# Performance work log

Measured on AMD Instinct MI355X. Metric: run time of the kernel, lower is better.

The kernel has to match this reference:

```python
import jax, jax.numpy as jnp
import numpy as np

B, N = 65536, 128

def setup_inputs() -> dict:
    key = jax.random.key(0)
    k1, k2, k3, k4, k5 = jax.random.split(key, 5)
    density = jax.random.uniform(k1, (B, N), dtype=jnp.float32) * 10.0   # nonneg densities
    deltas = jax.random.uniform(k2, (B, N), dtype=jnp.float32) * 0.05 + 1e-3  # positive step sizes
    zs = jnp.cumsum(deltas, axis=-1) + 2.0                               # monotone sample depths
    raw_rgbs = jax.random.uniform(k4, (B, N, 3), dtype=jnp.float32)
    raw_normals = jax.random.normal(k5, (B, N, 3), dtype=jnp.float32)
    return {"density": density, "deltas": deltas, "zs": zs,
            "raw_rgbs": raw_rgbs, "raw_normals": raw_normals}


def reference(density, deltas, zs, raw_rgbs, raw_normals):
    # alpha -> transmittance (exclusive cumprod) -> weight
    alpha = 1.0 - jnp.exp(-density * deltas)                 # [B, N]
    one_minus = 1.0 - alpha
    cp = jnp.cumprod(one_minus, axis=-1)                     # inclusive cumprod
    trans = jnp.concatenate([jnp.ones_like(cp[:, :1]), cp[:, :-1]], axis=-1)  # exclusive
    weight = alpha * trans                                   # [B, N]

    # composites
    rgb = jnp.einsum('bn,bnc->bc', weight, raw_rgbs)         # [B, 3]
    acc = jnp.sum(weight, axis=1, keepdims=True)             # [B, 1]
    depth = jnp.sum(weight * zs, axis=1, keepdims=True) / (acc + 1e-8)  # normalized
    normal = jnp.einsum('bn,bnc->bc', weight, raw_normals)   # [B, 3]

    # pack outputs: rgb(3) | depth(1) | normal(3) | acc(1) -> [B, 8]
    return jnp.concatenate([rgb, depth, normal, acc], axis=-1)
```

## Files before the change

### kernel.cpp

```cpp
#include <hip/hip_runtime.h>


constexpr int RAYS = 65536;
constexpr int NS   = 128;
constexpr int WPB  = 4;

#define DPP_ADD(x, ctrl, rm)                                                   \
    x += __int_as_float(__builtin_amdgcn_update_dpp(                           \
        0, __float_as_int(x), ctrl, rm, 0xf, true))

__device__ __forceinline__ float scan32(float x) {
    DPP_ADD(x, 0x111, 0xf);
    DPP_ADD(x, 0x112, 0xf);
    DPP_ADD(x, 0x114, 0xf);
    DPP_ADD(x, 0x118, 0xf);
    DPP_ADD(x, 0x142, 0xa);
    return x;
}

__global__ __launch_bounds__(256) void render_composite_kernel(
    const float* __restrict__ density,
    const float* __restrict__ deltas,
    const float* __restrict__ zs,
    const float* __restrict__ rgbs,
    const float* __restrict__ normals,
    float* __restrict__ out)
{
    __shared__ __align__(16) float wlds[WPB][256];

    const int tid  = threadIdx.x;
    const int wv   = tid >> 6;
    const int l    = tid & 63;
    const int k    = l & 31;
    const int half = l >> 5;

    const int ray0 = (blockIdx.x * WPB + wv) * 2;
    const int ray  = ray0 + half;

    const size_t row = (size_t)ray * NS;
    const float4 d  = reinterpret_cast<const float4*>(density + row)[k];
    const float4 dl = reinterpret_cast<const float4*>(deltas  + row)[k];
    const float4 z  = reinterpret_cast<const float4*>(zs      + row)[k];

    const float4* cr = reinterpret_cast<const float4*>(rgbs)    + (size_t)ray0 * 96;
    const float4* cn = reinterpret_cast<const float4*>(normals) + (size_t)ray0 * 96;
    const float4 vr0 = cr[0 * 64 + l];
    const float4 vr1 = cr[1 * 64 + l];
    const float4 vr2 = cr[2 * 64 + l];
    const float4 vn0 = cn[0 * 64 + l];
    const float4 vn1 = cn[1 * 64 + l];
    const float4 vn2 = cn[2 * 64 + l];

    const float s0 = d.x * dl.x;
    const float s1 = d.y * dl.y;
    const float s2 = d.z * dl.z;
    const float s3 = d.w * dl.w;
    const float slocal = (s0 + s1) + (s2 + s3);
    const float prefix = scan32(slocal);
    const float S0 = prefix - slocal;

    const float e0 = __expf(-S0);
    const float e1 = __expf(-(S0 + s0));
    const float e2 = __expf(-(S0 + s0 + s1));
    const float e3 = __expf(-(S0 + s0 + s1 + s2));
    const float e4 = __expf(-(S0 + slocal));
    const float w0 = e0 - e1, w1 = e1 - e2, w2 = e2 - e3, w3 = e3 - e4;

    float acc_w  = (w0 + w1) + (w2 + w3);
    float acc_wz = w0 * z.x + w1 * z.y + w2 * z.z + w3 * z.w;

    reinterpret_cast<float4*>(&wlds[wv][0])[l] = make_float4(w0, w1, w2, w3);
    const float* wbase = &wlds[wv][0];

    float r0c0 = 0.f, r0c1 = 0.f, r0c2 = 0.f;
    float r1c0 = 0.f, r1c1 = 0.f, r1c2 = 0.f;
    float m0c0 = 0.f, m0c1 = 0.f, m0c2 = 0.f;
    float m1c0 = 0.f, m1c1 = 0.f, m1c2 = 0.f;

    auto proc = [](const float4 v, float wA, float wB, int rt,
                   float& c0, float& c1, float& c2) {
        const float q0 = wA * v.x + wB * v.w;
        const float q1 = ((rt == 2) ? wB : wA) * v.y;
        const float q2 = ((rt >= 1) ? wB : wA) * v.z;
        const float a0 = (rt == 0) ? q0 : (rt == 1) ? q2 : q1;
        const float a1 = (rt == 0) ? q1 : (rt == 1) ? q0 : q2;
        const float a2 = (rt == 0) ? q2 : (rt == 1) ? q1 : q0;
        c0 += a0; c1 += a1; c2 += a2;
    };

    #pragma unroll
    for (int t = 0; t < 3; ++t) {
        const int f  = 256 * t + 4 * l;
        const int q  = f / 3;
        const int rt = f - 3 * q;
        const float wA = wbase[q];
        const float wB = wbase[q + 1];
        const float4 vr = (t == 0) ? vr0 : (t == 1) ? vr1 : vr2;
        const float4 vn = (t == 0) ? vn0 : (t == 1) ? vn1 : vn2;

        if (t == 0) {
            proc(vr, wA, wB, rt, r0c0, r0c1, r0c2);
            proc(vn, wA, wB, rt, m0c0, m0c1, m0c2);
        } else if (t == 2) {
            proc(vr, wA, wB, rt, r1c0, r1c1, r1c2);
            proc(vn, wA, wB, rt, m1c0, m1c1, m1c2);
        } else {
            float t0 = 0.f, t1c = 0.f, t2c = 0.f, u0 = 0.f, u1 = 0.f, u2 = 0.f;
            proc(vr, wA, wB, rt, t0, t1c, t2c);
            proc(vn, wA, wB, rt, u0, u1, u2);
            const bool isr0 = (l < 32);
            r0c0 += isr0 ? t0 : 0.f;  r1c0 += isr0 ? 0.f : t0;
            r0c1 += isr0 ? t1c : 0.f; r1c1 += isr0 ? 0.f : t1c;
            r0c2 += isr0 ? t2c : 0.f; r1c2 += isr0 ? 0.f : t2c;
            m0c0 += isr0 ? u0 : 0.f;  m1c0 += isr0 ? 0.f : u0;
            m0c1 += isr0 ? u1 : 0.f;  m1c1 += isr0 ? 0.f : u1;
            m0c2 += isr0 ? u2 : 0.f;  m1c2 += isr0 ? 0.f : u2;
        }
    }

    auto reduce2 = [&](float cR0, float cR1) -> float {
        const float sel = half ? cR1 : cR0;
        const float oth = half ? cR0 : cR1;
        const float m = sel + __shfl_xor(oth, 32, 64);
        return scan32(m);
    };
    const float R  = reduce2(r0c0, r1c0);
    const float G  = reduce2(r0c1, r1c1);
    const float Bc = reduce2(r0c2, r1c2);
    const float NR = reduce2(m0c0, m1c0);
    const float NG = reduce2(m0c1, m1c1);
    const float NB = reduce2(m0c2, m1c2);
    acc_w  = scan32(acc_w);
    acc_wz = scan32(acc_wz);

    if (k == 31) {
        const float depth = acc_wz / (acc_w + 1e-8f);
        float4* o = reinterpret_cast<float4*>(out + (size_t)ray * 8);
        o[0] = make_float4(R, G, Bc, depth);
        o[1] = make_float4(NR, NG, NB, acc_w);
    }
}

extern "C" void kernel_launch(void* const* d_in, const int* in_sizes, int n_in,
                              void* d_out, int out_size, void* d_ws, size_t ws_size,
                              hipStream_t stream) {
    const float* density = (const float*)d_in[0];
    const float* deltas  = (const float*)d_in[1];
    const float* zs      = (const float*)d_in[2];
    const float* rgbs    = (const float*)d_in[3];
    const float* normals = (const float*)d_in[4];
    float* out = (float*)d_out;

    const int grid = RAYS / (WPB * 2);
    render_composite_kernel<<<grid, 256, 0, stream>>>(
        density, deltas, zs, rgbs, normals, out);
}
```

Measured before the change: 279.7 us.

## Process four ray pairs per wave with double-buffered register prefetch

```diff
diff --git a/kernel.cpp b/kernel.cpp
--- a/kernel.cpp
+++ b/kernel.cpp
@@ -4,6 +4,10 @@
 constexpr int RAYS = 65536;
 constexpr int NS   = 128;
 constexpr int WPB  = 4;
+constexpr int NBLOCKS = 2048;
+constexpr int NWAVES  = NBLOCKS * WPB;
+constexpr int PAIRS   = RAYS / 2;
+constexpr int PPW     = PAIRS / NWAVES;
 
 #define DPP_ADD(x, ctrl, rm)                                                   \
     x += __int_as_float(__builtin_amdgcn_update_dpp(                           \
@@ -18,43 +22,37 @@
     return x;
 }
 
-__global__ __launch_bounds__(256) void render_composite_kernel(
-    const float* __restrict__ density,
-    const float* __restrict__ deltas,
-    const float* __restrict__ zs,
-    const float* __restrict__ rgbs,
-    const float* __restrict__ normals,
-    float* __restrict__ out)
+struct Stage {
+    float4 d, dl, z;
+    float4 r0, r1, r2;
+    float4 n0, n1, n2;
+};
+
+__device__ __forceinline__ void stage_load(
+    Stage& s, int pair, int l, int k,
+    const float* __restrict__ density, const float* __restrict__ deltas,
+    const float* __restrict__ zs, const float* __restrict__ rgbs,
+    const float* __restrict__ normals)
 {
-    __shared__ __align__(16) float wlds[WPB][256];
+    const int ray = pair * 2 + (l >> 5);
+    const size_t row = (size_t)ray * NS;
+    s.d  = reinterpret_cast<const float4*>(density + row)[k];
+    s.dl = reinterpret_cast<const float4*>(deltas  + row)[k];
+    s.z  = reinterpret_cast<const float4*>(zs      + row)[k];
+    const float4* cr = reinterpret_cast<const float4*>(rgbs)    + (size_t)pair * 192;
+    const float4* cn = reinterpret_cast<const float4*>(normals) + (size_t)pair * 192;
+    s.r0 = cr[l]; s.r1 = cr[64 + l]; s.r2 = cr[128 + l];
+    s.n0 = cn[l]; s.n1 = cn[64 + l]; s.n2 = cn[128 + l];
+}
 
-    const int tid  = threadIdx.x;
-    const int wv   = tid >> 6;
-    const int l    = tid & 63;
-    const int k    = l & 31;
-    const int half = l >> 5;
-
-    const int ray0 = (blockIdx.x * WPB + wv) * 2;
-    const int ray  = ray0 + half;
-
-    const size_t row = (size_t)ray * NS;
-    const float4 d  = reinterpret_cast<const float4*>(density + row)[k];
-    const float4 dl = reinterpret_cast<const float4*>(deltas  + row)[k];
-    const float4 z  = reinterpret_cast<const float4*>(zs      + row)[k];
-
-    const float4* cr = reinterpret_cast<const float4*>(rgbs)    + (size_t)ray0 * 96;
-    const float4* cn = reinterpret_cast<const float4*>(normals) + (size_t)ray0 * 96;
-    const float4 vr0 = cr[0 * 64 + l];
-    const float4 vr1 = cr[1 * 64 + l];
-    const float4 vr2 = cr[2 * 64 + l];
-    const float4 vn0 = cn[0 * 64 + l];
-    const float4 vn1 = cn[1 * 64 + l];
-    const float4 vn2 = cn[2 * 64 + l];
-
-    const float s0 = d.x * dl.x;
-    const float s1 = d.y * dl.y;
-    const float s2 = d.z * dl.z;
-    const float s3 = d.w * dl.w;
+__device__ __forceinline__ void compute_pair(
+    const Stage& s, int pair, int l, int k, int half,
+    float* wbase, float* __restrict__ out)
+{
+    const float s0 = s.d.x * s.dl.x;
+    const float s1 = s.d.y * s.dl.y;
+    const float s2 = s.d.z * s.dl.z;
+    const float s3 = s.d.w * s.dl.w;
     const float slocal = (s0 + s1) + (s2 + s3);
     const float prefix = scan32(slocal);
     const float S0 = prefix - slocal;
@@ -67,10 +65,9 @@
     const float w0 = e0 - e1, w1 = e1 - e2, w2 = e2 - e3, w3 = e3 - e4;
 
     float acc_w  = (w0 + w1) + (w2 + w3);
-    float acc_wz = w0 * z.x + w1 * z.y + w2 * z.z + w3 * z.w;
+    float acc_wz = w0 * s.z.x + w1 * s.z.y + w2 * s.z.z + w3 * s.z.w;
 
-    reinterpret_cast<float4*>(&wlds[wv][0])[l] = make_float4(w0, w1, w2, w3);
-    const float* wbase = &wlds[wv][0];
+    reinterpret_cast<float4*>(wbase)[l] = make_float4(w0, w1, w2, w3);
 
     float r0c0 = 0.f, r0c1 = 0.f, r0c2 = 0.f;
     float r1c0 = 0.f, r1c1 = 0.f, r1c2 = 0.f;
@@ -95,8 +92,8 @@
         const int rt = f - 3 * q;
         const float wA = wbase[q];
         const float wB = wbase[q + 1];
-        const float4 vr = (t == 0) ? vr0 : (t == 1) ? vr1 : vr2;
-        const float4 vn = (t == 0) ? vn0 : (t == 1) ? vn1 : vn2;
+        const float4 vr = (t == 0) ? s.r0 : (t == 1) ? s.r1 : s.r2;
+        const float4 vn = (t == 0) ? s.n0 : (t == 1) ? s.n1 : s.n2;
 
         if (t == 0) {
             proc(vr, wA, wB, rt, r0c0, r0c1, r0c2);
@@ -134,11 +131,40 @@
     acc_wz = scan32(acc_wz);
 
     if (k == 31) {
+        const int ray = pair * 2 + half;
         const float depth = acc_wz / (acc_w + 1e-8f);
         float4* o = reinterpret_cast<float4*>(out + (size_t)ray * 8);
         o[0] = make_float4(R, G, Bc, depth);
         o[1] = make_float4(NR, NG, NB, acc_w);
     }
+}
+
+__global__ __launch_bounds__(256, 4) void render_composite_kernel(
+    const float* __restrict__ density, const float* __restrict__ deltas,
+    const float* __restrict__ zs, const float* __restrict__ rgbs,
+    const float* __restrict__ normals, float* __restrict__ out)
+{
+    __shared__ __align__(16) float wlds[WPB][256];
+
+    const int tid  = threadIdx.x;
+    const int wv   = tid >> 6;
+    const int l    = tid & 63;
+    const int k    = l & 31;
+    const int half = l >> 5;
+    float* wbase = &wlds[wv][0];
+
+    const int gw = blockIdx.x * WPB + wv;
+    const int p0 = gw * PPW;
+
+    Stage A, B;
+    stage_load(A, p0 + 0, l, k, density, deltas, zs, rgbs, normals);
+    stage_load(B, p0 + 1, l, k, density, deltas, zs, rgbs, normals);
+    compute_pair(A, p0 + 0, l, k, half, wbase, out);
+    stage_load(A, p0 + 2, l, k, density, deltas, zs, rgbs, normals);
+    compute_pair(B, p0 + 1, l, k, half, wbase, out);
+    stage_load(B, p0 + 3, l, k, density, deltas, zs, rgbs, normals);
+    compute_pair(A, p0 + 2, l, k, half, wbase, out);
+    compute_pair(B, p0 + 3, l, k, half, wbase, out);
 }
 
 extern "C" void kernel_launch(void* const* d_in, const int* in_sizes, int n_in,
@@ -151,7 +177,6 @@
     const float* normals = (const float*)d_in[4];
     float* out = (float*)d_out;
 
-    const int grid = RAYS / (WPB * 2);
-    render_composite_kernel<<<grid, 256, 0, stream>>>(
+    render_composite_kernel<<<NBLOCKS, 256, 0, stream>>>(
         density, deltas, zs, rgbs, normals, out);
 }
```

Result: no change. 283.6 us (+1.4%).
